# Performance work log

Measured on AMD Instinct MI355X. Metric: run time of the kernel, lower is better.

Reference implementation:

```python
import jax, jax.numpy as jnp
import numpy as np

N_NODES = 50000
N_EDGES = 600000
F_IN = 128
DIM_H = 256
N_CLASSES = 40
BN_EPS = 1e-5


def setup_inputs() -> dict:
    key = jax.random.key(0)
    ks = jax.random.split(key, 10)
    x = jax.random.normal(ks[0], (N_NODES, F_IN), dtype=jnp.float32)
    edge_index = jax.random.randint(ks[1], (2, N_EDGES), 0, N_NODES, dtype=jnp.int64)
    s1 = 1.0 / np.sqrt(F_IN)
    s2 = 1.0 / np.sqrt(DIM_H)
    W1 = jax.random.uniform(ks[2], (F_IN, DIM_H), jnp.float32, -s1, s1)
    b1 = jax.random.uniform(ks[3], (DIM_H,), jnp.float32, -s1, s1)
    gamma = jnp.ones((DIM_H,), jnp.float32)
    beta = jnp.zeros((DIM_H,), jnp.float32)
    W2 = jax.random.uniform(ks[4], (DIM_H, DIM_H), jnp.float32, -s2, s2)
    b2 = jax.random.uniform(ks[5], (DIM_H,), jnp.float32, -s2, s2)
    Wlin = jax.random.uniform(ks[6], (DIM_H, N_CLASSES), jnp.float32, -s2, s2)
    blin = jax.random.uniform(ks[7], (N_CLASSES,), jnp.float32, -s2, s2)
    return {"x": x, "edge_index": edge_index, "W1": W1, "b1": b1,
            "gamma": gamma, "beta": beta, "W2": W2, "b2": b2,
            "Wlin": Wlin, "blin": blin}


def reference(x, edge_index, W1, b1, gamma, beta, W2, b2, Wlin, blin):
    src, dst = edge_index[0], edge_index[1]
    # GIN sum aggregation: agg[i] = sum_{(j->i)} x[j]; eps = 0 (default)
    agg = jax.ops.segment_sum(x[src], dst, num_segments=N_NODES)  # [N, F_IN]
    h = x + agg
    # MLP: Linear -> BatchNorm1d (training-mode batch stats) -> ReLU -> Linear -> ReLU
    h = h @ W1 + b1                               # [N, DIM_H]
    mean = jnp.mean(h, axis=0)
    var = jnp.var(h, axis=0)                      # biased, as torch BN uses for normalization
    h = (h - mean) * jax.lax.rsqrt(var + BN_EPS) * gamma + beta
    h = jax.nn.relu(h)
    h = jax.nn.relu(h @ W2 + b2)                  # MLP final ReLU; outer x.relu() is idempotent
    return h @ Wlin + blin                        # [N, N_CLASSES]
```

## Files before the change

### kernel.cpp

```cpp
#include <hip/hip_runtime.h>

#define F_IN 128
#define DIM_H 256
#define N_CLASSES 40
#define BN_EPS 1e-5f
#define M_PAD 50176

typedef short bf16x8 __attribute__((ext_vector_type(8)));
typedef float f32x4 __attribute__((ext_vector_type(4)));

__device__ __forceinline__ unsigned short f2bf(float f) {
    union { float f; unsigned u; } v; v.f = f;
    unsigned r = v.u + 0x7fff + ((v.u >> 16) & 1);
    return (unsigned short)(r >> 16);
}
__device__ __forceinline__ float bf2f(unsigned short u) {
    union { unsigned u; float f; } v; v.u = ((unsigned)u) << 16;
    return v.f;
}
__device__ __forceinline__ float4 bf2f4(ushort4 u) {
    return make_float4(bf2f(u.x), bf2f(u.y), bf2f(u.z), bf2f(u.w));
}

__global__ void hist_kernel(const int* __restrict__ dst, int* __restrict__ hist, int nE) {
    int e = blockIdx.x * blockDim.x + threadIdx.x;
    if (e >= nE) return;
    atomicAdd(&hist[dst[e]], 1);
}

__global__ void scan_blocks_kernel(const int* __restrict__ hist,
                                   int* __restrict__ blockSums, int M) {
    __shared__ int lds[256];
    int t = threadIdx.x;
    int i = blockIdx.x * 256 + t;
    lds[t] = (i < M) ? hist[i] : 0;
    __syncthreads();
    for (int off = 128; off > 0; off >>= 1) {
        if (t < off) lds[t] += lds[t + off];
        __syncthreads();
    }
    if (t == 0) blockSums[blockIdx.x] = lds[0];
}

__global__ void scan_offsets_kernel(const int* __restrict__ blockSums,
                                    int* __restrict__ blockOffs,
                                    int nB, int* __restrict__ start, int M, int nE) {
    __shared__ int lds[256];
    int t = threadIdx.x;
    int orig = (t < nB) ? blockSums[t] : 0;
    lds[t] = orig;
    __syncthreads();
    for (int off = 1; off < 256; off <<= 1) {
        int v = (t >= off) ? lds[t - off] : 0;
        __syncthreads();
        lds[t] += v;
        __syncthreads();
    }
    if (t < nB) blockOffs[t] = lds[t] - orig;
    if (t == 0) start[M] = nE;
}

__global__ void scan_final_kernel(const int* __restrict__ hist,
                                  const int* __restrict__ blockOffs,
                                  int* __restrict__ start, int M) {
    __shared__ int lds[256];
    int t = threadIdx.x;
    int i = blockIdx.x * 256 + t;
    int orig = (i < M) ? hist[i] : 0;
    lds[t] = orig;
    __syncthreads();
    for (int off = 1; off < 256; off <<= 1) {
        int v = (t >= off) ? lds[t - off] : 0;
        __syncthreads();
        lds[t] += v;
        __syncthreads();
    }
    if (i < M) start[i] = blockOffs[blockIdx.x] + lds[t] - orig;
}

__global__ void fill_kernel(const int* __restrict__ src, const int* __restrict__ dst,
                            const int* __restrict__ start, int* __restrict__ cursor,
                            int* __restrict__ order, int nE) {
    int e = blockIdx.x * blockDim.x + threadIdx.x;
    if (e >= nE) return;
    int d = dst[e];
    int pos = start[d] + atomicAdd(&cursor[d], 1);
    order[pos] = src[e];
}

__global__ void prep_kernel(const float* __restrict__ x, unsigned short* __restrict__ xb,
                            const float* __restrict__ W1, const float* __restrict__ W2,
                            const float* __restrict__ Wl,
                            unsigned short* __restrict__ W1t,
                            unsigned short* __restrict__ W2t,
                            unsigned short* __restrict__ Wlt,
                            unsigned short* __restrict__ h1pad,
                            int XQ) {
    int idx = blockIdx.x * 256 + threadIdx.x;
    if (idx < XQ) {
        float4 v = ((const float4*)x)[idx];
        ushort4 o;
        o.x = f2bf(v.x); o.y = f2bf(v.y); o.z = f2bf(v.z); o.w = f2bf(v.w);
        ((ushort4*)xb)[idx] = o;
        return;
    }
    int j = idx - XQ;
    if (j < 32768) {
        int n = j >> 7, k = j & 127;
        W1t[j] = f2bf(W1[k * DIM_H + n]);
    } else if (j < 32768 + 65536) {
        int i = j - 32768;
        int n = i >> 8, k = i & 255;
        W2t[i] = f2bf(W2[k * DIM_H + n]);
    } else if (j < 32768 + 65536 + 16384) {
        int i = j - 98304;
        int n = i >> 8, k = i & 255;
        Wlt[i] = f2bf((n < N_CLASSES) ? Wl[k * N_CLASSES + n] : 0.f);
    } else if (j < 114688 + 3072) {
        int i = j - 114688;
        ((ushort4*)h1pad)[i] = make_ushort4(0, 0, 0, 0);
    }
}

__global__ void bn_reduce_kernel(const float* __restrict__ partials, int R,
                                 const float* __restrict__ gamma,
                                 const float* __restrict__ beta,
                                 float* __restrict__ scale,
                                 float* __restrict__ shift, int M) {
    __shared__ float ls[256], lss[256];
    int c = blockIdx.x, t = threadIdx.x;
    float s = 0.f, ss = 0.f;
    for (int r = t; r < R; r += 256) {
        s += partials[(long)r * 512 + c];
        ss += partials[(long)r * 512 + 256 + c];
    }
    ls[t] = s; lss[t] = ss;
    __syncthreads();
    for (int o = 128; o > 0; o >>= 1) {
        if (t < o) { ls[t] += ls[t + o]; lss[t] += lss[t + o]; }
        __syncthreads();
    }
    if (t == 0) {
        float inv = 1.0f / (float)M;
        float mean = ls[0] * inv;
        float var = lss[0] * inv - mean * mean;
        float sc = gamma[c] * rsqrtf(var + BN_EPS);
        scale[c] = sc;
        shift[c] = beta[c] - mean * sc;
    }
}

__global__ __launch_bounds__(256, 4) void gin_gemm1_kernel(
    const float* __restrict__ x, const unsigned short* __restrict__ xb,
    const int* __restrict__ order, const int* __restrict__ start,
    const unsigned short* __restrict__ W1t, const float* __restrict__ b1,
    unsigned short* __restrict__ h1, float* __restrict__ partials, int M) {
    constexpr int K = F_IN, S = K / 32;
    constexpr int PA = 136;
    constexpr int PB = 40;
    __shared__ __align__(16) unsigned short At[64 * PA];
    __shared__ __align__(16) unsigned short Bs[256 * PB];

    int tid = threadIdx.x;
    int wave = tid >> 6, lane = tid & 63;
    int l15 = lane & 15, q = lane >> 4;
    int wn = wave;
    long row0 = (long)blockIdx.x * 64;

    bf16x8 br[4];
    auto loadB = [&](int s) {
#pragma unroll
        for (int i = 0; i < 4; ++i) {
            int ch = tid + i * 256;
            int m = ch >> 2, c = ch & 3;
            br[i] = *(const bf16x8*)(W1t + m * K + s * 32 + c * 8);
        }
    };
    auto writeB = [&]() {
#pragma unroll
        for (int i = 0; i < 4; ++i) {
            int ch = tid + i * 256;
            int m = ch >> 2, c = ch & 3;
            *(bf16x8*)(&Bs[m * PB + c * 8]) = br[i];
        }
    };

    loadB(0);

    {
        int hw = tid >> 5, lane32 = tid & 31;
        const ushort4* xv = (const ushort4*)xb;
        for (int rr = 0; rr < 8; ++rr) {
            int r = rr * 8 + hw;
            long node = row0 + r;
            float4 a0 = make_float4(0.f, 0.f, 0.f, 0.f);
            float4 a1 = a0, a2 = a0, a3 = a0;
            if (node < M) {
                a0 = ((const float4*)x)[node * 32 + lane32];
                int e0 = start[node], e1 = start[node + 1];
                int e = e0;
                for (; e + 4 <= e1; e += 4) {
                    int s0 = order[e], s1 = order[e + 1], s2 = order[e + 2], s3 = order[e + 3];
                    float4 v0 = bf2f4(xv[(size_t)s0 * 32 + lane32]);
                    float4 v1 = bf2f4(xv[(size_t)s1 * 32 + lane32]);
                    float4 v2 = bf2f4(xv[(size_t)s2 * 32 + lane32]);
                    float4 v3 = bf2f4(xv[(size_t)s3 * 32 + lane32]);
                    a0.x += v0.x; a0.y += v0.y; a0.z += v0.z; a0.w += v0.w;
                    a1.x += v1.x; a1.y += v1.y; a1.z += v1.z; a1.w += v1.w;
                    a2.x += v2.x; a2.y += v2.y; a2.z += v2.z; a2.w += v2.w;
                    a3.x += v3.x; a3.y += v3.y; a3.z += v3.z; a3.w += v3.w;
                }
                for (; e < e1; ++e) {
                    float4 v = bf2f4(xv[(size_t)order[e] * 32 + lane32]);
                    a1.x += v.x; a1.y += v.y; a1.z += v.z; a1.w += v.w;
                }
            }
            float4 t;
            t.x = (a0.x + a1.x) + (a2.x + a3.x);
            t.y = (a0.y + a1.y) + (a2.y + a3.y);
            t.z = (a0.z + a1.z) + (a2.z + a3.z);
            t.w = (a0.w + a1.w) + (a2.w + a3.w);
            ushort4 o;
            o.x = f2bf(t.x); o.y = f2bf(t.y); o.z = f2bf(t.z); o.w = f2bf(t.w);
            *(ushort4*)(&At[r * PA + lane32 * 4]) = o;
        }
    }
    writeB();
    __syncthreads();

    f32x4 acc[4][4] = {};
#pragma unroll
    for (int s = 0; s < S; ++s) {
        if (s + 1 < S) loadB(s + 1);
        bf16x8 af[4], bfr[4];
#pragma unroll
        for (int mt = 0; mt < 4; ++mt)
            af[mt] = *(const bf16x8*)(&At[(mt * 16 + l15) * PA + s * 32 + q * 8]);
#pragma unroll
        for (int nt = 0; nt < 4; ++nt)
            bfr[nt] = *(const bf16x8*)(&Bs[(wn * 64 + nt * 16 + l15) * PB + q * 8]);
#pragma unroll
        for (int mt = 0; mt < 4; ++mt)
#pragma unroll
            for (int nt = 0; nt < 4; ++nt)
                acc[mt][nt] = __builtin_amdgcn_mfma_f32_16x16x32_bf16(
                    af[mt], bfr[nt], acc[mt][nt], 0, 0, 0);
        __syncthreads();
        if (s + 1 < S) { writeB(); __syncthreads(); }
    }

#pragma unroll
    for (int nt = 0; nt < 4; ++nt) {
        int col = wn * 64 + nt * 16 + l15;
        float b = b1[col];
        float s = 0.f, ss = 0.f;
#pragma unroll
        for (int mt = 0; mt < 4; ++mt) {
#pragma unroll
            for (int r = 0; r < 4; ++r) {
                long row = row0 + mt * 16 + q * 4 + r;
                float v = acc[mt][nt][r] + b;
                if (row < M) {
                    h1[row * DIM_H + col] = f2bf(v);
                    s += v; ss += v * v;
                }
            }
        }
        s += __shfl_xor(s, 16, 64);  s += __shfl_xor(s, 32, 64);
        ss += __shfl_xor(ss, 16, 64); ss += __shfl_xor(ss, 32, 64);
        if (lane < 16) {
            partials[(long)blockIdx.x * 512 + col] = s;
            partials[(long)blockIdx.x * 512 + 256 + col] = ss;
        }
    }
}

__global__ __launch_bounds__(256, 4) void gemm23_kernel(
    const unsigned short* __restrict__ h1, const unsigned short* __restrict__ W2t,
    const float* __restrict__ b2,
    const float* __restrict__ scale, const float* __restrict__ shift,
    const unsigned short* __restrict__ Wlt, const float* __restrict__ blin,
    float* __restrict__ out, int M) {
    constexpr int K = DIM_H, S = K / 32;
    constexpr int PA = 40;
    constexpr int PB = 40;
    constexpr int PH = 264;
    constexpr int LDSN = 64 * PH;
    __shared__ __align__(16) unsigned short lds[LDSN];
    unsigned short* As = lds;
    unsigned short* Bs = lds + 64 * PA;
    unsigned short* h2t = lds;

    int tid = threadIdx.x;
    int wave = tid >> 6, lane = tid & 63;
    int l15 = lane & 15, q = lane >> 4;
    int wn = wave;
    long row0 = (long)blockIdx.x * 64;

    bf16x8 ar, br[4];
    auto loadAB = [&](int s) {
        {
            int m = tid >> 2, c = tid & 3;
            ar = *(const bf16x8*)(h1 + (row0 + m) * K + s * 32 + c * 8);
        }
#pragma unroll
        for (int i = 0; i < 4; ++i) {
            int ch = tid + i * 256;
            int m = ch >> 2, c = ch & 3;
            br[i] = *(const bf16x8*)(W2t + m * K + s * 32 + c * 8);
        }
    };
    auto writeAB = [&](int s) {
        {
            int m = tid >> 2, c = tid & 3;
            int kb = s * 32 + c * 8;
            float4 sc0 = *(const float4*)(scale + kb);
            float4 sc1 = *(const float4*)(scale + kb + 4);
            float4 sh0 = *(const float4*)(shift + kb);
            float4 sh1 = *(const float4*)(shift + kb + 4);
            float scv[8] = {sc0.x, sc0.y, sc0.z, sc0.w, sc1.x, sc1.y, sc1.z, sc1.w};
            float shv[8] = {sh0.x, sh0.y, sh0.z, sh0.w, sh1.x, sh1.y, sh1.z, sh1.w};
            bf16x8 v = ar;
#pragma unroll
            for (int j = 0; j < 8; ++j) {
                float f = bf2f((unsigned short)v[j]);
                f = fmaxf(f * scv[j] + shv[j], 0.f);
                v[j] = (short)f2bf(f);
            }
            *(bf16x8*)(&As[m * PA + c * 8]) = v;
        }
#pragma unroll
        for (int i = 0; i < 4; ++i) {
            int ch = tid + i * 256;
            int m = ch >> 2, c = ch & 3;
            *(bf16x8*)(&Bs[m * PB + c * 8]) = br[i];
        }
    };

    f32x4 acc[4][4] = {};

    loadAB(0);
    writeAB(0);
    __syncthreads();
#pragma unroll
    for (int s = 0; s < S; ++s) {
        if (s + 1 < S) loadAB(s + 1);
        bf16x8 af[4], bfr[4];
#pragma unroll
        for (int mt = 0; mt < 4; ++mt)
            af[mt] = *(const bf16x8*)(&As[(mt * 16 + l15) * PA + q * 8]);
#pragma unroll
        for (int nt = 0; nt < 4; ++nt)
            bfr[nt] = *(const bf16x8*)(&Bs[(wn * 64 + nt * 16 + l15) * PB + q * 8]);
#pragma unroll
        for (int mt = 0; mt < 4; ++mt)
#pragma unroll
            for (int nt = 0; nt < 4; ++nt)
                acc[mt][nt] = __builtin_amdgcn_mfma_f32_16x16x32_bf16(
                    af[mt], bfr[nt], acc[mt][nt], 0, 0, 0);
        __syncthreads();
        if (s + 1 < S) { writeAB(s + 1); __syncthreads(); }
    }

#pragma unroll
    for (int nt = 0; nt < 4; ++nt) {
        int colL = wn * 64 + nt * 16 + l15;
        float b = b2[colL];
#pragma unroll
        for (int mt = 0; mt < 4; ++mt)
#pragma unroll
            for (int r = 0; r < 4; ++r) {
                int rowL = mt * 16 + q * 4 + r;
                h2t[rowL * PH + colL] = f2bf(fmaxf(acc[mt][nt][r] + b, 0.f));
            }
    }
    __syncthreads();

    f32x4 acc3[3] = {};
#pragma unroll
    for (int s = 0; s < 8; ++s) {
        bf16x8 a3 = *(const bf16x8*)(&h2t[(wave * 16 + l15) * PH + s * 32 + q * 8]);
#pragma unroll
        for (int nt = 0; nt < 3; ++nt) {
            bf16x8 b3 = *(const bf16x8*)(Wlt + (nt * 16 + l15) * 256 + s * 32 + q * 8);
            acc3[nt] = __builtin_amdgcn_mfma_f32_16x16x32_bf16(a3, b3, acc3[nt], 0, 0, 0);
        }
    }
#pragma unroll
    for (int nt = 0; nt < 3; ++nt) {
        int col = nt * 16 + l15;
        if (col < N_CLASSES) {
            float b = blin[col];
#pragma unroll
            for (int r = 0; r < 4; ++r) {
                long row = row0 + wave * 16 + q * 4 + r;
                if (row < M) out[row * N_CLASSES + col] = acc3[nt][r] + b;
            }
        }
    }
}

extern "C" void kernel_launch(void* const* d_in, const int* in_sizes, int n_in,
                              void* d_out, int out_size, void* d_ws, size_t ws_size,
                              hipStream_t stream) {
    const float* x     = (const float*)d_in[0];
    const int*   ei    = (const int*)d_in[1];
    const float* W1    = (const float*)d_in[2];
    const float* b1    = (const float*)d_in[3];
    const float* gamma = (const float*)d_in[4];
    const float* beta  = (const float*)d_in[5];
    const float* W2    = (const float*)d_in[6];
    const float* b2    = (const float*)d_in[7];
    const float* Wlin  = (const float*)d_in[8];
    const float* blin  = (const float*)d_in[9];
    float* out = (float*)d_out;

    int M  = in_sizes[0] / F_IN;
    int nE = in_sizes[1] / 2;
    const int* srcIdx = ei;
    const int* dstIdx = ei + nE;
    int nB = (M + 255) / 256;
    int gy = (M + 63) / 64;
    int XQ = M * 32;

    unsigned short* h1bf  = (unsigned short*)d_ws;
    unsigned short* xb    = h1bf + (size_t)M_PAD * DIM_H;
    unsigned short* W1t   = xb + (size_t)M_PAD * F_IN;
    unsigned short* W2t   = W1t + DIM_H * F_IN;
    unsigned short* Wlt   = W2t + DIM_H * DIM_H;
    float*          partials = (float*)(Wlt + 64 * DIM_H);
    float*          scale = partials + (size_t)800 * 512;
    float*          shift = scale + DIM_H;
    int*            hist  = (int*)(shift + DIM_H);
    int*            cursor= hist + M;
    int*            start = cursor + M;
    int*            blockSums = start + (M + 1);
    int*            blockOffs = blockSums + 256;
    int*            order = blockOffs + 256;

    hipMemsetAsync(hist, 0, (size_t)2 * M * sizeof(int), stream);

    int tB = 256;
    hist_kernel<<<(nE + tB - 1) / tB, tB, 0, stream>>>(dstIdx, hist, nE);
    scan_blocks_kernel<<<nB, 256, 0, stream>>>(hist, blockSums, M);
    scan_offsets_kernel<<<1, 256, 0, stream>>>(blockSums, blockOffs, nB, start, M, nE);
    scan_final_kernel<<<nB, 256, 0, stream>>>(hist, blockOffs, start, M);
    fill_kernel<<<(nE + tB - 1) / tB, tB, 0, stream>>>(srcIdx, dstIdx, start, cursor, order, nE);
    prep_kernel<<<(XQ + 114688 + 3072 + 255) / 256, 256, 0, stream>>>(
        x, xb, W1, W2, Wlin, W1t, W2t, Wlt, h1bf + (size_t)M * DIM_H, XQ);

    gin_gemm1_kernel<<<gy, 256, 0, stream>>>(x, xb, order, start, W1t, b1, h1bf, partials, M);
    bn_reduce_kernel<<<DIM_H, 256, 0, stream>>>(partials, gy, gamma, beta, scale, shift, M);
    gemm23_kernel<<<gy, 256, 0, stream>>>(h1bf, W2t, b2, scale, shift, Wlt, blin, out, M);
}
```

Before: 247.5 us.

## Retile second GEMM to 128 rows, stage h1 stores, trim scan and memset launches

Several changes land together. gemm23 now uses 512-thread blocks over 128-row tiles with double-buffered LDS and one barrier per k-step. gemm1 stages its h1 output through LDS for coalesced 16-byte stores and reads the self term from the bf16 copy of x instead of fp32. The scan drops its separate offsets kernel by having each block reduce the preceding block sums itself, and the histogram memset is folded into prep_kernel, which now runs first. This cuts kernel launches and global traffic, at the cost of more LDS per block, lower precision on the self term, and h1 padding rows that are written with computed values instead of zeros.

```diff
diff --git a/kernel.cpp b/kernel.cpp
--- a/kernel.cpp
+++ b/kernel.cpp
@@ -42,40 +42,31 @@
     if (t == 0) blockSums[blockIdx.x] = lds[0];
 }
 
-__global__ void scan_offsets_kernel(const int* __restrict__ blockSums,
-                                    int* __restrict__ blockOffs,
-                                    int nB, int* __restrict__ start, int M, int nE) {
+__global__ void scan_final_kernel(const int* __restrict__ hist,
+                                  const int* __restrict__ blockSums,
+                                  int* __restrict__ start, int M, int nE) {
     __shared__ int lds[256];
     int t = threadIdx.x;
-    int orig = (t < nB) ? blockSums[t] : 0;
-    lds[t] = orig;
-    __syncthreads();
-    for (int off = 1; off < 256; off <<= 1) {
-        int v = (t >= off) ? lds[t - off] : 0;
-        __syncthreads();
-        lds[t] += v;
-        __syncthreads();
-    }
-    if (t < nB) blockOffs[t] = lds[t] - orig;
-    if (t == 0) start[M] = nE;
-}
-
-__global__ void scan_final_kernel(const int* __restrict__ hist,
-                                  const int* __restrict__ blockOffs,
-                                  int* __restrict__ start, int M) {
-    __shared__ int lds[256];
-    int t = threadIdx.x;
+    lds[t] = (t < blockIdx.x) ? blockSums[t] : 0;
+    __syncthreads();
+    for (int o = 128; o > 0; o >>= 1) {
+        if (t < o) lds[t] += lds[t + o];
+        __syncthreads();
+    }
+    int off = lds[0];
+    __syncthreads();
     int i = blockIdx.x * 256 + t;
     int orig = (i < M) ? hist[i] : 0;
     lds[t] = orig;
     __syncthreads();
-    for (int off = 1; off < 256; off <<= 1) {
-        int v = (t >= off) ? lds[t - off] : 0;
+    for (int o = 1; o < 256; o <<= 1) {
+        int v = (t >= o) ? lds[t - o] : 0;
         __syncthreads();
         lds[t] += v;
         __syncthreads();
     }
-    if (i < M) start[i] = blockOffs[blockIdx.x] + lds[t] - orig;
+    if (i < M) start[i] = off + lds[t] - orig;
+    if (blockIdx.x == 0 && t == 0) start[M] = nE;
 }
 
 __global__ void fill_kernel(const int* __restrict__ src, const int* __restrict__ dst,
@@ -94,8 +85,8 @@
                             unsigned short* __restrict__ W1t,
                             unsigned short* __restrict__ W2t,
                             unsigned short* __restrict__ Wlt,
-                            unsigned short* __restrict__ h1pad,
-                            int XQ) {
+                            int* __restrict__ histz,
+                            int XQ, int ZQ) {
     int idx = blockIdx.x * 256 + threadIdx.x;
     if (idx < XQ) {
         float4 v = ((const float4*)x)[idx];
@@ -116,9 +107,11 @@
         int i = j - 98304;
         int n = i >> 8, k = i & 255;
         Wlt[i] = f2bf((n < N_CLASSES) ? Wl[k * N_CLASSES + n] : 0.f);
-    } else if (j < 114688 + 3072) {
-        int i = j - 114688;
-        ((ushort4*)h1pad)[i] = make_ushort4(0, 0, 0, 0);
+    } else if (j < 114688 + 0 + 1) {
+    }
+    int z = j - 114688;
+    if (z >= 0 && z < ZQ) {
+        ((int4*)histz)[z] = make_int4(0, 0, 0, 0);
     }
 }
 
@@ -151,15 +144,18 @@
 }
 
 __global__ __launch_bounds__(256, 4) void gin_gemm1_kernel(
-    const float* __restrict__ x, const unsigned short* __restrict__ xb,
+    const unsigned short* __restrict__ xb,
     const int* __restrict__ order, const int* __restrict__ start,
     const unsigned short* __restrict__ W1t, const float* __restrict__ b1,
     unsigned short* __restrict__ h1, float* __restrict__ partials, int M) {
     constexpr int K = F_IN, S = K / 32;
     constexpr int PA = 136;
     constexpr int PB = 40;
-    __shared__ __align__(16) unsigned short At[64 * PA];
-    __shared__ __align__(16) unsigned short Bs[256 * PB];
+    constexpr int PH = 264;
+    __shared__ __align__(16) unsigned short lds[64 * PA + 256 * PB];
+    unsigned short* At = lds;
+    unsigned short* Bs = lds + 64 * PA;
+    unsigned short* h1t = lds;
 
     int tid = threadIdx.x;
     int wave = tid >> 6, lane = tid & 63;
@@ -196,7 +192,7 @@
             float4 a0 = make_float4(0.f, 0.f, 0.f, 0.f);
             float4 a1 = a0, a2 = a0, a3 = a0;
             if (node < M) {
-                a0 = ((const float4*)x)[node * 32 + lane32];
+                a0 = bf2f4(xv[node * 32 + lane32]);
                 int e0 = start[node], e1 = start[node + 1];
                 int e = e0;
                 for (; e + 4 <= e1; e += 4) {
@@ -260,10 +256,8 @@
             for (int r = 0; r < 4; ++r) {
                 long row = row0 + mt * 16 + q * 4 + r;
                 float v = acc[mt][nt][r] + b;
-                if (row < M) {
-                    h1[row * DIM_H + col] = f2bf(v);
-                    s += v; ss += v * v;
-                }
+                if (row < M) { s += v; ss += v * v; }
+                h1t[(mt * 16 + q * 4 + r) * PH + col] = f2bf(v);
             }
         }
         s += __shfl_xor(s, 16, 64);  s += __shfl_xor(s, 32, 64);
@@ -273,47 +267,51 @@
             partials[(long)blockIdx.x * 512 + 256 + col] = ss;
         }
     }
-}
-
-__global__ __launch_bounds__(256, 4) void gemm23_kernel(
+    __syncthreads();
+    {
+        int srow = tid >> 2, scol = (tid & 3) * 64;
+        unsigned short* dst = h1 + (row0 + srow) * DIM_H + scol;
+        const unsigned short* srcp = &h1t[srow * PH + scol];
+#pragma unroll
+        for (int j = 0; j < 8; ++j)
+            *(bf16x8*)(dst + j * 8) = *(const bf16x8*)(srcp + j * 8);
+    }
+}
+
+__global__ __launch_bounds__(512, 4) void gemm23_kernel(
     const unsigned short* __restrict__ h1, const unsigned short* __restrict__ W2t,
     const float* __restrict__ b2,
     const float* __restrict__ scale, const float* __restrict__ shift,
     const unsigned short* __restrict__ Wlt, const float* __restrict__ blin,
     float* __restrict__ out, int M) {
-    constexpr int K = DIM_H, S = K / 32;
-    constexpr int PA = 40;
-    constexpr int PB = 40;
-    constexpr int PH = 264;
-    constexpr int LDSN = 64 * PH;
-    __shared__ __align__(16) unsigned short lds[LDSN];
-    unsigned short* As = lds;
-    unsigned short* Bs = lds + 64 * PA;
+    constexpr int S = 8;
+    constexpr int PA = 40, PB = 40, PH = 264;
+    constexpr int STAGE = 128 * PA + 256 * PB;
+    __shared__ __align__(16) unsigned short lds[128 * PH];
     unsigned short* h2t = lds;
 
     int tid = threadIdx.x;
     int wave = tid >> 6, lane = tid & 63;
+    int wm = wave >> 2, wn = wave & 3;
     int l15 = lane & 15, q = lane >> 4;
-    int wn = wave;
-    long row0 = (long)blockIdx.x * 64;
-
-    bf16x8 ar, br[4];
+    long row0 = (long)blockIdx.x * 128;
+
+    int am = tid >> 2, ac = tid & 3;
+    bf16x8 ar, br[2];
     auto loadAB = [&](int s) {
+        ar = *(const bf16x8*)(h1 + (row0 + am) * DIM_H + s * 32 + ac * 8);
+#pragma unroll
+        for (int i = 0; i < 2; ++i) {
+            int ch = tid + i * 512;
+            int m = ch >> 2, c = ch & 3;
+            br[i] = *(const bf16x8*)(W2t + m * DIM_H + s * 32 + c * 8);
+        }
+    };
+    auto writeAB = [&](int s, int buf) {
+        unsigned short* As = lds + buf * STAGE;
+        unsigned short* Bs = As + 128 * PA;
         {
-            int m = tid >> 2, c = tid & 3;
-            ar = *(const bf16x8*)(h1 + (row0 + m) * K + s * 32 + c * 8);
-        }
-#pragma unroll
-        for (int i = 0; i < 4; ++i) {
-            int ch = tid + i * 256;
-            int m = ch >> 2, c = ch & 3;
-            br[i] = *(const bf16x8*)(W2t + m * K + s * 32 + c * 8);
-        }
-    };
-    auto writeAB = [&](int s) {
-        {
-            int m = tid >> 2, c = tid & 3;
-            int kb = s * 32 + c * 8;
+            int kb = s * 32 + ac * 8;
             float4 sc0 = *(const float4*)(scale + kb);
             float4 sc1 = *(const float4*)(scale + kb + 4);
             float4 sh0 = *(const float4*)(shift + kb);
@@ -327,28 +325,29 @@
                 f = fmaxf(f * scv[j] + shv[j], 0.f);
                 v[j] = (short)f2bf(f);
             }
-            *(bf16x8*)(&As[m * PA + c * 8]) = v;
-        }
-#pragma unroll
-        for (int i = 0; i < 4; ++i) {
-            int ch = tid + i * 256;
+            *(bf16x8*)(&As[am * PA + ac * 8]) = v;
+        }
+#pragma unroll
+        for (int i = 0; i < 2; ++i) {
+            int ch = tid + i * 512;
             int m = ch >> 2, c = ch & 3;
             *(bf16x8*)(&Bs[m * PB + c * 8]) = br[i];
         }
     };
 
     f32x4 acc[4][4] = {};
-
     loadAB(0);
-    writeAB(0);
-    __syncthreads();
+    writeAB(0, 0);
 #pragma unroll
     for (int s = 0; s < S; ++s) {
         if (s + 1 < S) loadAB(s + 1);
+        __syncthreads();
+        const unsigned short* As = lds + (s & 1) * STAGE;
+        const unsigned short* Bs = As + 128 * PA;
         bf16x8 af[4], bfr[4];
 #pragma unroll
         for (int mt = 0; mt < 4; ++mt)
-            af[mt] = *(const bf16x8*)(&As[(mt * 16 + l15) * PA + q * 8]);
+            af[mt] = *(const bf16x8*)(&As[(wm * 64 + mt * 16 + l15) * PA + q * 8]);
 #pragma unroll
         for (int nt = 0; nt < 4; ++nt)
             bfr[nt] = *(const bf16x8*)(&Bs[(wn * 64 + nt * 16 + l15) * PB + q * 8]);
@@ -358,9 +357,9 @@
             for (int nt = 0; nt < 4; ++nt)
                 acc[mt][nt] = __builtin_amdgcn_mfma_f32_16x16x32_bf16(
                     af[mt], bfr[nt], acc[mt][nt], 0, 0, 0);
-        __syncthreads();
-        if (s + 1 < S) { writeAB(s + 1); __syncthreads(); }
-    }
+        if (s + 1 < S) writeAB(s + 1, (s + 1) & 1);
+    }
+    __syncthreads();
 
 #pragma unroll
     for (int nt = 0; nt < 4; ++nt) {
@@ -370,7 +369,7 @@
         for (int mt = 0; mt < 4; ++mt)
 #pragma unroll
             for (int r = 0; r < 4; ++r) {
-                int rowL = mt * 16 + q * 4 + r;
+                int rowL = wm * 64 + mt * 16 + q * 4 + r;
                 h2t[rowL * PH + colL] = f2bf(fmaxf(acc[mt][nt][r] + b, 0.f));
             }
     }
@@ -420,8 +419,10 @@
     const int* srcIdx = ei;
     const int* dstIdx = ei + nE;
     int nB = (M + 255) / 256;
-    int gy = (M + 63) / 64;
+    int gy1 = (M + 63) / 64;
+    int gy23 = (M + 127) / 128;
     int XQ = M * 32;
+    int ZQ = 2 * M / 4;
 
     unsigned short* h1bf  = (unsigned short*)d_ws;
     unsigned short* xb    = h1bf + (size_t)M_PAD * DIM_H;
@@ -435,21 +436,17 @@
     int*            cursor= hist + M;
     int*            start = cursor + M;
     int*            blockSums = start + (M + 1);
-    int*            blockOffs = blockSums + 256;
-    int*            order = blockOffs + 256;
-
-    hipMemsetAsync(hist, 0, (size_t)2 * M * sizeof(int), stream);
+    int*            order = blockSums + 256;
 
     int tB = 256;
+    prep_kernel<<<(XQ + 114688 + ZQ + 255) / 256, 256, 0, stream>>>(
+        x, xb, W1, W2, Wlin, W1t, W2t, Wlt, hist, XQ, ZQ);
     hist_kernel<<<(nE + tB - 1) / tB, tB, 0, stream>>>(dstIdx, hist, nE);
     scan_blocks_kernel<<<nB, 256, 0, stream>>>(hist, blockSums, M);
-    scan_offsets_kernel<<<1, 256, 0, stream>>>(blockSums, blockOffs, nB, start, M, nE);
-    scan_final_kernel<<<nB, 256, 0, stream>>>(hist, blockOffs, start, M);
+    scan_final_kernel<<<nB, 256, 0, stream>>>(hist, blockSums, start, M, nE);
     fill_kernel<<<(nE + tB - 1) / tB, tB, 0, stream>>>(srcIdx, dstIdx, start, cursor, order, nE);
-    prep_kernel<<<(XQ + 114688 + 3072 + 255) / 256, 256, 0, stream>>>(
-        x, xb, W1, W2, Wlin, W1t, W2t, Wlt, h1bf + (size_t)M * DIM_H, XQ);
-
-    gin_gemm1_kernel<<<gy, 256, 0, stream>>>(x, xb, order, start, W1t, b1, h1bf, partials, M);
-    bn_reduce_kernel<<<DIM_H, 256, 0, stream>>>(partials, gy, gamma, beta, scale, shift, M);
-    gemm23_kernel<<<gy, 256, 0, stream>>>(h1bf, W2t, b2, scale, shift, Wlt, blin, out, M);
-}
+
+    gin_gemm1_kernel<<<gy1, 256, 0, stream>>>(xb, order, start, W1t, b1, h1bf, partials, M);
+    bn_reduce_kernel<<<DIM_H, 256, 0, stream>>>(partials, gy1, gamma, beta, scale, shift, M);
+    gemm23_kernel<<<gy23, 512, 0, stream>>>(h1bf, W2t, b2, scale, shift, Wlt, blin, out, M);
+}
```

Measured after the change: 241.5 us. 2.4% less time.
